# Optimization experiments

Measured on AMD Instinct MI355X. Metric: run time of the kernel, lower is better.

The kernel has to match this reference:

```python
import jax, jax.numpy as jnp
import numpy as np

TAU = 0.2
EPS_NORM = 1e-12  # torch F.normalize eps


def _l2_normalize(x):
    n = jnp.linalg.norm(x, axis=-1, keepdims=True)
    return x / jnp.maximum(n, EPS_NORM)


def setup_inputs() -> dict:
    key = jax.random.key(0)
    k1, k2 = jax.random.split(key)
    seg_emb = jax.random.normal(k1, (131072, 512), dtype=jnp.float32)
    prototypes = jax.random.normal(k2, (64, 512), dtype=jnp.float32) * 0.02
    return {"seg_emb": seg_emb, "prototypes": prototypes}


def reference(seg_emb, prototypes):
    # normalize -> cosine-sim matmul -> temperature scale -> softmax -> weighted proto sum
    p = _l2_normalize(prototypes)          # [K, D]
    z = _l2_normalize(seg_emb)             # [N, D]
    logits = jnp.einsum('nd,kd->nk', z, p) / max(TAU, 1e-06)  # [N, K]
    w = jax.nn.softmax(logits, axis=-1)    # [N, K]
    pattern = jnp.einsum('nk,kd->nd', w, prototypes)           # [N, D]
    return pattern, w, logits
```

## Files before the change

### kernel.cpp

```cpp
#include <hip/hip_runtime.h>
#include <hip/hip_bf16.h>

typedef __attribute__((ext_vector_type(8))) short short8;
typedef __attribute__((ext_vector_type(4))) float f32x4;

#define NPROTO 64
#define DIM    512
#define TAU_INV 5.0f

__device__ __forceinline__ unsigned short f2bf(float f) {
    union { float f; unsigned int u; } v; v.f = f;
    unsigned int r = v.u + 0x7FFFu + ((v.u >> 16) & 1u);
    return (unsigned short)(r >> 16);
}

__global__ void pb_prep(const float* __restrict__ protos,
                        unsigned short* __restrict__ pnorm,
                        unsigned short* __restrict__ protosT) {
    const int k    = blockIdx.x;
    const int lane = threadIdx.x;
    const float* row = protos + k * DIM;
    float x[8];
    float ss = 0.0f;
#pragma unroll
    for (int j = 0; j < 8; ++j) {
        x[j] = row[lane * 8 + j];
        ss += x[j] * x[j];
    }
#pragma unroll
    for (int m = 1; m < 64; m <<= 1) ss += __shfl_xor(ss, m, 64);
    const float s = 1.0f / fmaxf(sqrtf(ss), 1e-12f);
    short8 pn;
#pragma unroll
    for (int j = 0; j < 8; ++j) pn[j] = (short)f2bf(x[j] * s);
    *reinterpret_cast<short8*>(pnorm + k * DIM + lane * 8) = pn;
#pragma unroll
    for (int j = 0; j < 8; ++j)
        protosT[(lane * 8 + j) * NPROTO + k] = f2bf(x[j]);
}

__global__ __launch_bounds__(256, 8) void pb_main(
    const float* __restrict__ seg,
    const unsigned short* __restrict__ pnorm,
    const unsigned short* __restrict__ protosT,
    float* __restrict__ out_pat,
    float* __restrict__ out_w,
    float* __restrict__ out_log) {

    __shared__ unsigned short wbuf_all[4 * 16 * 64];

    const int wid  = (int)(threadIdx.x >> 6);
    const int lane = (int)(threadIdx.x & 63);
    const int g    = lane >> 4;
    const int r16  = lane & 15;
    const long n0  = ((long)blockIdx.x * 4 + wid) * 16;

    f32x4 acc[4] = {};
    float ss = 0.0f;
    const float* aptr = seg + (n0 + r16) * DIM + g * 8;
#pragma unroll 4
    for (int kt = 0; kt < 16; ++kt) {
        const f32x4 a0 = *reinterpret_cast<const f32x4*>(aptr + kt * 32);
        const f32x4 a1 = *reinterpret_cast<const f32x4*>(aptr + kt * 32 + 4);
        short8 af;
#pragma unroll
        for (int j = 0; j < 4; ++j) {
            ss += a0[j] * a0[j];
            ss += a1[j] * a1[j];
            af[j]     = (short)f2bf(a0[j]);
            af[j + 4] = (short)f2bf(a1[j]);
        }
#pragma unroll
        for (int c = 0; c < 4; ++c) {
            const short8 bf = *reinterpret_cast<const short8*>(
                pnorm + (c * 16 + r16) * DIM + g * 8 + kt * 32);
            acc[c] = __builtin_amdgcn_mfma_f32_16x16x32_bf16(af, bf, acc[c], 0, 0, 0);
        }
    }

    ss += __shfl_xor(ss, 16, 64);
    ss += __shfl_xor(ss, 32, 64);
    const float sc_own = TAU_INV / fmaxf(sqrtf(ss), 1e-12f);
    float sc[4];
#pragma unroll
    for (int q = 0; q < 4; ++q) sc[q] = __shfl(sc_own, g * 4 + q, 64);

    float lg[4][4];
#pragma unroll
    for (int c = 0; c < 4; ++c)
#pragma unroll
        for (int q = 0; q < 4; ++q) {
            lg[c][q] = acc[c][q] * sc[q];
            out_log[(n0 + g * 4 + q) * NPROTO + c * 16 + r16] = lg[c][q];
        }

    float w[4][4];
#pragma unroll
    for (int q = 0; q < 4; ++q) {
        float mx = fmaxf(fmaxf(lg[0][q], lg[1][q]), fmaxf(lg[2][q], lg[3][q]));
#pragma unroll
        for (int msk = 1; msk < 16; msk <<= 1) mx = fmaxf(mx, __shfl_xor(mx, msk, 64));
        const float e0 = __expf(lg[0][q] - mx);
        const float e1 = __expf(lg[1][q] - mx);
        const float e2 = __expf(lg[2][q] - mx);
        const float e3 = __expf(lg[3][q] - mx);
        float sum = e0 + e1 + e2 + e3;
#pragma unroll
        for (int msk = 1; msk < 16; msk <<= 1) sum += __shfl_xor(sum, msk, 64);
        const float inv = 1.0f / sum;
        w[0][q] = e0 * inv; w[1][q] = e1 * inv; w[2][q] = e2 * inv; w[3][q] = e3 * inv;
    }

    unsigned short* wb = wbuf_all + wid * (16 * 64);
#pragma unroll
    for (int c = 0; c < 4; ++c)
#pragma unroll
        for (int q = 0; q < 4; ++q) {
            out_w[(n0 + g * 4 + q) * NPROTO + c * 16 + r16] = w[c][q];
            const int row  = g * 4 + q;
            const int col  = c * 16 + r16;
            const int byte = (row * 128 + col * 2) ^ ((row & 7) << 4);
            *reinterpret_cast<unsigned short*>(reinterpret_cast<char*>(wb) + byte) =
                f2bf(w[c][q]);
        }

    __syncthreads();

    short8 wa0, wa1;
    {
        const int row = r16;
        const int b0 = (row * 128 + g * 16)      ^ ((row & 7) << 4);
        const int b1 = (row * 128 + g * 16 + 64) ^ ((row & 7) << 4);
        wa0 = *reinterpret_cast<const short8*>(reinterpret_cast<char*>(wb) + b0);
        wa1 = *reinterpret_cast<const short8*>(reinterpret_cast<char*>(wb) + b1);
    }

#pragma unroll 2
    for (int cp = 0; cp < 32; ++cp) {
        const unsigned short* bp = protosT + (cp * 16 + r16) * NPROTO + g * 8;
        const short8 b0 = *reinterpret_cast<const short8*>(bp);
        const short8 b1 = *reinterpret_cast<const short8*>(bp + 32);
        f32x4 pacc = {};
        pacc = __builtin_amdgcn_mfma_f32_16x16x32_bf16(wa0, b0, pacc, 0, 0, 0);
        pacc = __builtin_amdgcn_mfma_f32_16x16x32_bf16(wa1, b1, pacc, 0, 0, 0);
#pragma unroll
        for (int q = 0; q < 4; ++q)
            out_pat[(n0 + g * 4 + q) * DIM + cp * 16 + r16] = pacc[q];
    }
}

extern "C" void kernel_launch(void* const* d_in, const int* in_sizes, int n_in,
                              void* d_out, int out_size, void* d_ws, size_t ws_size,
                              hipStream_t stream) {
    const float* seg    = (const float*)d_in[0];
    const float* protos = (const float*)d_in[1];
    const int N = in_sizes[0] / DIM;

    float* out     = (float*)d_out;
    float* out_pat = out;
    float* out_w   = out_pat + (size_t)N * DIM;
    float* out_log = out_w + (size_t)N * NPROTO;

    unsigned short* pnorm   = (unsigned short*)d_ws;
    unsigned short* protosT = pnorm + NPROTO * DIM;

    pb_prep<<<NPROTO, 64, 0, stream>>>(protos, pnorm, protosT);
    pb_main<<<N / 64, 256, 0, stream>>>(seg, pnorm, protosT, out_pat, out_w, out_log);
}
```

Baseline: 179.3 us.

## Stage normalized prototypes in swizzled LDS with 1024-thread blocks

Grows each block to 16 waves (1024 threads) and has the whole block cooperatively copy the bf16 normalized prototype matrix (64 KB) into LDS with an XOR swizzle, so the first MFMA loop reads B fragments from LDS instead of global/L2. The same LDS buffer is then reused for the per-wave softmax weight tiles after a barrier. This trades fewer global prototype reads for a 64 KB LDS footprint per block, which limits how many blocks fit per CU, plus extra block-wide barriers. The kernel is heavily store-bound on its outputs, so occupancy loss may matter.

Result: slower. 188.4 us (+5.1%).

```diff
diff --git a/kernel.cpp b/kernel.cpp
--- a/kernel.cpp
+++ b/kernel.cpp
@@ -39,7 +39,7 @@
         protosT[(lane * 8 + j) * NPROTO + k] = f2bf(x[j]);
 }
 
-__global__ __launch_bounds__(256, 8) void pb_main(
+__global__ __launch_bounds__(1024, 8) void pb_main(
     const float* __restrict__ seg,
     const unsigned short* __restrict__ pnorm,
     const unsigned short* __restrict__ protosT,
@@ -47,13 +47,24 @@
     float* __restrict__ out_w,
     float* __restrict__ out_log) {
 
-    __shared__ unsigned short wbuf_all[4 * 16 * 64];
+    __shared__ char lds[65536];
 
-    const int wid  = (int)(threadIdx.x >> 6);
-    const int lane = (int)(threadIdx.x & 63);
+    const int tid  = (int)threadIdx.x;
+    const int wid  = tid >> 6;
+    const int lane = tid & 63;
     const int g    = lane >> 4;
     const int r16  = lane & 15;
-    const long n0  = ((long)blockIdx.x * 4 + wid) * 16;
+    const long n0  = ((long)blockIdx.x * 16 + wid) * 16;
+
+#pragma unroll
+    for (int pass = 0; pass < 4; ++pass) {
+        const int G  = tid + pass * 1024;
+        const int p  = G >> 6;
+        const int gi = G & 63;
+        const short8 v = *reinterpret_cast<const short8*>(pnorm + p * DIM + gi * 8);
+        *reinterpret_cast<short8*>(lds + p * 1024 + ((gi ^ (p & 15)) << 4)) = v;
+    }
+    __syncthreads();
 
     f32x4 acc[4] = {};
     float ss = 0.0f;
@@ -70,10 +81,11 @@
             af[j]     = (short)f2bf(a0[j]);
             af[j + 4] = (short)f2bf(a1[j]);
         }
+        const int gidx = (kt * 4 + g) ^ r16;
 #pragma unroll
         for (int c = 0; c < 4; ++c) {
             const short8 bf = *reinterpret_cast<const short8*>(
-                pnorm + (c * 16 + r16) * DIM + g * 8 + kt * 32);
+                lds + (c * 16 + r16) * 1024 + (gidx << 4));
             acc[c] = __builtin_amdgcn_mfma_f32_16x16x32_bf16(af, bf, acc[c], 0, 0, 0);
         }
     }
@@ -111,7 +123,9 @@
         w[0][q] = e0 * inv; w[1][q] = e1 * inv; w[2][q] = e2 * inv; w[3][q] = e3 * inv;
     }
 
-    unsigned short* wb = wbuf_all + wid * (16 * 64);
+    __syncthreads();
+
+    char* wb = lds + wid * 2048;
 #pragma unroll
     for (int c = 0; c < 4; ++c)
 #pragma unroll
@@ -120,19 +134,15 @@
             const int row  = g * 4 + q;
             const int col  = c * 16 + r16;
             const int byte = (row * 128 + col * 2) ^ ((row & 7) << 4);
-            *reinterpret_cast<unsigned short*>(reinterpret_cast<char*>(wb) + byte) =
-                f2bf(w[c][q]);
+            *reinterpret_cast<unsigned short*>(wb + byte) = f2bf(w[c][q]);
         }
-
-    __syncthreads();
 
     short8 wa0, wa1;
     {
-        const int row = r16;
-        const int b0 = (row * 128 + g * 16)      ^ ((row & 7) << 4);
-        const int b1 = (row * 128 + g * 16 + 64) ^ ((row & 7) << 4);
-        wa0 = *reinterpret_cast<const short8*>(reinterpret_cast<char*>(wb) + b0);
-        wa1 = *reinterpret_cast<const short8*>(reinterpret_cast<char*>(wb) + b1);
+        const int b0 = (r16 * 128 + g * 16)      ^ ((r16 & 7) << 4);
+        const int b1 = (r16 * 128 + g * 16 + 64) ^ ((r16 & 7) << 4);
+        wa0 = *reinterpret_cast<const short8*>(wb + b0);
+        wa1 = *reinterpret_cast<const short8*>(wb + b1);
     }
 
 #pragma unroll 2
@@ -165,5 +175,5 @@
     unsigned short* protosT = pnorm + NPROTO * DIM;
 
     pb_prep<<<NPROTO, 64, 0, stream>>>(protos, pnorm, protosT);
-    pb_main<<<N / 64, 256, 0, stream>>>(seg, pnorm, protosT, out_pat, out_w, out_log);
+    pb_main<<<N / 256, 1024, 0, stream>>>(seg, pnorm, protosT, out_pat, out_w, out_log);
 }
```
